# Kernel optimization log

Hardware: AMD Instinct MI355X
Metric: run time of the kernel (lower is better)

## Reference

```python
import jax, jax.numpy as jnp
import numpy as np

N_EMBED = 1024
HEAD_SIZE = 128

def setup_inputs() -> dict:
    key = jax.random.key(0)
    k1, k2, k3, k4 = jax.random.split(key, 4)
    x = jax.random.normal(k1, (8, 2048, N_EMBED), dtype=jnp.float32)
    # torch.nn.Linear default init: U(-1/sqrt(in), 1/sqrt(in)); stored as [out, in],
    # we store transposed [in, out] for x @ W.
    bound = 1.0 / np.sqrt(N_EMBED)
    Wk = jax.random.uniform(k2, (N_EMBED, HEAD_SIZE), jnp.float32, -bound, bound)
    Wq = jax.random.uniform(k3, (N_EMBED, HEAD_SIZE), jnp.float32, -bound, bound)
    Wv = jax.random.uniform(k4, (N_EMBED, HEAD_SIZE), jnp.float32, -bound, bound)
    return {"x": x, "Wk": Wk, "Wq": Wq, "Wv": Wv}

def reference(x, Wk, Wq, Wv):
    # x: [B, T, E]
    k = jnp.einsum('bte,eh->bth', x, Wk)  # [B, T, H]
    q = jnp.einsum('bte,eh->bth', x, Wq)
    v = jnp.einsum('bte,eh->bth', x, Wv)
    scale = 1.0 / np.sqrt(HEAD_SIZE).astype(np.float32)
    wei = jnp.einsum('bqh,bkh->bqk', q, k) * scale  # [B, T, T]
    wei = jax.nn.softmax(wei, axis=-1)
    out = jnp.einsum('bqk,bkh->bqh', wei, v)  # [B, T, H]
    return out
```

## Files before the change

### kernel.cpp

```cpp
#include <hip/hip_runtime.h>

#define BATCH 8
#define TLEN 2048
#define EMB 1024
#define HDIM 128
#define SCALE 0.08838834764831845f
#define NSPLIT 4

typedef _Float16 f16x8 __attribute__((ext_vector_type(8)));
typedef _Float16 f16x4 __attribute__((ext_vector_type(4)));
typedef float f32x4 __attribute__((ext_vector_type(4)));

static __device__ __forceinline__ f32x4 mfma16(f16x8 a, f16x8 b, f32x4 c) {
    return __builtin_amdgcn_mfma_f32_16x16x32_f16(a, b, c, 0, 0, 0);
}

__global__ void prep_w(const float* __restrict__ Wk, const float* __restrict__ Wq,
                       const float* __restrict__ Wv, _Float16* __restrict__ wtf) {
    int g = blockIdx.x * 256 + threadIdx.x;
    int lane = g & 63;
    int kstep = (g >> 6) & 31;
    int ntile = g >> 11;
    int n = ntile * 16 + (lane & 15);
    int sel = n >> 7;
    int h = n & 127;
    const float* W = (sel == 0) ? Wk : (sel == 1) ? Wq : Wv;
    int kbase = kstep * 32 + (lane >> 4) * 8;
    f16x8 o;
#pragma unroll
    for (int j = 0; j < 8; j++) {
        float v = W[(size_t)(kbase + j) * HDIM + h];
        if (sel == 1) v *= SCALE;
        o[j] = (_Float16)v;
    }
    *(f16x8*)&wtf[(size_t)g * 8] = o;
}

__global__ __launch_bounds__(256, 2) void proj_kernel(
        const float* __restrict__ x, const _Float16* __restrict__ wtf,
        _Float16* __restrict__ kb, _Float16* __restrict__ qb, _Float16* __restrict__ vbT) {
    __shared__ _Float16 xs[2][32 * 72];
    const int t = threadIdx.x;
    const int m0 = blockIdx.x * 32;
    const int wv = t >> 6;
    const int lane = t & 63;
    const int m16 = lane & 15;
    const int quad = lane >> 4;
    const int n0 = wv * 96;
    const int r0 = t >> 4;
    const int c0 = (t & 15) * 4;

    const f32x4 zero4 = {0.f, 0.f, 0.f, 0.f};
    f32x4 acc[2][6];
#pragma unroll
    for (int mt = 0; mt < 2; mt++)
#pragma unroll
        for (int nt = 0; nt < 6; nt++) acc[mt][nt] = zero4;

    const float* xrow0 = &x[(size_t)(m0 + r0) * EMB + c0];
    const float* xrow1 = &x[(size_t)(m0 + 16 + r0) * EMB + c0];

    float4 xv[2][2];
    f16x8 bf[2][12];
    xv[0][0] = *(const float4*)(xrow0);
    xv[0][1] = *(const float4*)(xrow1);
#pragma unroll
    for (int ks = 0; ks < 2; ks++)
#pragma unroll
        for (int nt = 0; nt < 6; nt++)
            bf[0][ks * 6 + nt] = *(const f16x8*)
                &wtf[((size_t)((wv * 6 + nt) * 32 + ks) * 64 + lane) * 8];

#pragma unroll
    for (int it = 0; it < 16; it++) {
        const int cur = it & 1, nxt = cur ^ 1;
#pragma unroll
        for (int i = 0; i < 2; i++) {
            f16x4 h;
            h[0] = (_Float16)xv[cur][i].x; h[1] = (_Float16)xv[cur][i].y;
            h[2] = (_Float16)xv[cur][i].z; h[3] = (_Float16)xv[cur][i].w;
            *(f16x4*)&xs[cur][(r0 + 16 * i) * 72 + c0] = h;
        }
        __syncthreads();
        if (it < 15) {
            xv[nxt][0] = *(const float4*)(xrow0 + (it + 1) * 64);
            xv[nxt][1] = *(const float4*)(xrow1 + (it + 1) * 64);
#pragma unroll
            for (int ks = 0; ks < 2; ks++)
#pragma unroll
                for (int nt = 0; nt < 6; nt++)
                    bf[nxt][ks * 6 + nt] = *(const f16x8*)
                        &wtf[((size_t)((wv * 6 + nt) * 32 + (it + 1) * 2 + ks) * 64 + lane) * 8];
        }
#pragma unroll
        for (int ks = 0; ks < 2; ks++) {
            f16x8 a0 = *(const f16x8*)&xs[cur][m16 * 72 + ks * 32 + quad * 8];
            f16x8 a1 = *(const f16x8*)&xs[cur][(16 + m16) * 72 + ks * 32 + quad * 8];
#pragma unroll
            for (int nt = 0; nt < 6; nt++) {
                acc[0][nt] = mfma16(a0, bf[cur][ks * 6 + nt], acc[0][nt]);
                acc[1][nt] = mfma16(a1, bf[cur][ks * 6 + nt], acc[1][nt]);
            }
        }
    }
#pragma unroll
    for (int nt = 0; nt < 6; nt++) {
        int n = n0 + nt * 16 + m16;
        int nsel = n >> 7;
        int h = n & 127;
        if (nsel < 2) {
            _Float16* dst = (nsel == 0) ? kb : qb;
#pragma unroll
            for (int mt = 0; mt < 2; mt++)
#pragma unroll
                for (int r = 0; r < 4; r++) {
                    int mg = m0 + mt * 16 + quad * 4 + r;
                    dst[(size_t)mg * HDIM + h] = (_Float16)acc[mt][nt][r];
                }
        } else {
#pragma unroll
            for (int mt = 0; mt < 2; mt++) {
                int mg = m0 + mt * 16 + quad * 4;
                int bb = mg >> 11, tok = mg & 2047;
                f16x4 pk;
#pragma unroll
                for (int r = 0; r < 4; r++) pk[r] = (_Float16)acc[mt][nt][r];
                *(f16x4*)&vbT[((size_t)bb * HDIM + h) * TLEN + tok] = pk;
            }
        }
    }
}

__global__ __launch_bounds__(256, 3) void attn_kernel(
        const _Float16* __restrict__ qb, const _Float16* __restrict__ kb,
        const _Float16* __restrict__ vbT,
        _Float16* __restrict__ po, float* __restrict__ pl) {
    __shared__ _Float16 kls[64 * 132];
    __shared__ _Float16 vtl[128 * 68];
    __shared__ _Float16 pls[4 * 32 * 72];
    const int t = threadIdx.x;
    const int qt = blockIdx.x;
    const int b = blockIdx.y;
    const int sp = blockIdx.z;
    const int wv = t >> 6;
    const int lane = t & 63;
    const int m16 = lane & 15;
    const int quad = lane >> 4;
    const int q0 = qt * 128 + wv * 32;
    _Float16* pw = pls + wv * (32 * 72);

    f16x8 qf[2][4];
#pragma unroll
    for (int mt = 0; mt < 2; mt++)
#pragma unroll
        for (int ks = 0; ks < 4; ks++)
            qf[mt][ks] = *(const f16x8*)
                &qb[((size_t)b * TLEN + q0 + mt * 16 + m16) * HDIM + ks * 32 + quad * 8];

    const f32x4 zero4 = {0.f, 0.f, 0.f, 0.f};
    f32x4 o[2][8];
    float lacc[2] = {0.f, 0.f};
#pragma unroll
    for (int mt = 0; mt < 2; mt++)
#pragma unroll
        for (int nt = 0; nt < 8; nt++) o[mt][nt] = zero4;

    for (int kt = sp * 8; kt < sp * 8 + 8; kt++) {
        const int k0 = kt * 64;
        f16x8 kreg[4];
#pragma unroll
        for (int rep = 0; rep < 4; rep++) {
            int u = t + rep * 256;
            kreg[rep] = *(const f16x8*)
                &kb[((size_t)b * TLEN + k0 + (u >> 4)) * HDIM + (u & 15) * 8];
        }
        __syncthreads();
#pragma unroll
        for (int rep = 0; rep < 4; rep++) {
            int u = t + rep * 256;
            *(f16x8*)&kls[(u >> 4) * 132 + (u & 15) * 8] = kreg[rep];
        }
#pragma unroll
        for (int rep = 0; rep < 4; rep++) {
            int u = t + rep * 256;
            f16x8 v = *(const f16x8*)
                &vbT[((size_t)b * HDIM + (u >> 3)) * TLEN + k0 + (u & 7) * 8];
            *(f16x8*)&vtl[(u >> 3) * 68 + (u & 7) * 8] = v;
        }
        __syncthreads();
#pragma unroll
        for (int kt_ = 0; kt_ < 4; kt_++) {
            f32x4 st0 = zero4, st1 = zero4;
#pragma unroll
            for (int ks = 0; ks < 4; ks++) {
                f16x8 kf = *(const f16x8*)&kls[(kt_ * 16 + m16) * 132 + ks * 32 + quad * 8];
                st0 = mfma16(kf, qf[0][ks], st0);
                st1 = mfma16(kf, qf[1][ks], st1);
            }
            f16x4 p0, p1;
#pragma unroll
            for (int r = 0; r < 4; r++) {
                float e0 = __expf(st0[r]);
                float e1 = __expf(st1[r]);
                lacc[0] += e0;
                lacc[1] += e1;
                p0[r] = (_Float16)e0;
                p1[r] = (_Float16)e1;
            }
            *(f16x4*)&pw[m16 * 72 + kt_ * 16 + quad * 4] = p0;
            *(f16x4*)&pw[(16 + m16) * 72 + kt_ * 16 + quad * 4] = p1;
        }
        f16x8 ap[2][2];
#pragma unroll
        for (int mt = 0; mt < 2; mt++)
#pragma unroll
            for (int kc = 0; kc < 2; kc++)
                ap[mt][kc] = *(const f16x8*)&pw[(mt * 16 + m16) * 72 + kc * 32 + quad * 8];
#pragma unroll
        for (int nt = 0; nt < 8; nt++) {
            f16x8 b0 = *(const f16x8*)&vtl[(nt * 16 + m16) * 68 + quad * 8];
            f16x8 b1 = *(const f16x8*)&vtl[(nt * 16 + m16) * 68 + 32 + quad * 8];
            o[0][nt] = mfma16(ap[0][0], b0, o[0][nt]);
            o[0][nt] = mfma16(ap[0][1], b1, o[0][nt]);
            o[1][nt] = mfma16(ap[1][0], b0, o[1][nt]);
            o[1][nt] = mfma16(ap[1][1], b1, o[1][nt]);
        }
    }
#pragma unroll
    for (int mt = 0; mt < 2; mt++) {
        lacc[mt] += __shfl_xor(lacc[mt], 16);
        lacc[mt] += __shfl_xor(lacc[mt], 32);
    }
#pragma unroll
    for (int mt = 0; mt < 2; mt++) {
        if (quad == 0)
            pl[((size_t)(sp * BATCH + b)) * TLEN + q0 + mt * 16 + m16] = lacc[mt];
#pragma unroll
        for (int r = 0; r < 4; r++) {
            int row = q0 + mt * 16 + quad * 4 + r;
            size_t prow = ((size_t)(sp * BATCH + b)) * TLEN + row;
#pragma unroll
            for (int nt = 0; nt < 8; nt++)
                po[prow * HDIM + nt * 16 + m16] = (_Float16)o[mt][nt][r];
        }
    }
}

__global__ void combine_kernel(const _Float16* __restrict__ po, const float* __restrict__ pl,
                               float* __restrict__ out) {
    int g = blockIdx.x * 256 + threadIdx.x;
    int row = g >> 5;
    int part = g & 31;
    int bb = row >> 11;
    int tok = row & 2047;
    float L = 0.f;
    float4 acc = {0.f, 0.f, 0.f, 0.f};
#pragma unroll
    for (int s = 0; s < NSPLIT; s++) {
        size_t prow = ((size_t)(s * BATCH + bb)) * TLEN + tok;
        L += pl[prow];
        f16x4 p = *(const f16x4*)&po[prow * HDIM + part * 4];
        acc.x += (float)p[0]; acc.y += (float)p[1];
        acc.z += (float)p[2]; acc.w += (float)p[3];
    }
    float inv = 1.f / L;
    float4 res = {acc.x * inv, acc.y * inv, acc.z * inv, acc.w * inv};
    *(float4*)&out[(size_t)row * HDIM + part * 4] = res;
}

extern "C" void kernel_launch(void* const* d_in, const int* in_sizes, int n_in,
                              void* d_out, int out_size, void* d_ws, size_t ws_size,
                              hipStream_t stream) {
    const float* x  = (const float*)d_in[0];
    const float* Wk = (const float*)d_in[1];
    const float* Wq = (const float*)d_in[2];
    const float* Wv = (const float*)d_in[3];
    float* out = (float*)d_out;
    char* ws = (char*)d_ws;
    _Float16* wtf = (_Float16*)(ws);
    _Float16* kb  = (_Float16*)(ws + (1ull << 20));
    _Float16* qb  = (_Float16*)(ws + (5ull << 20));
    _Float16* vbT = (_Float16*)(ws + (9ull << 20));
    _Float16* po  = (_Float16*)(ws + (13ull << 20));
    float* pl = (float*)(ws + (29ull << 20));

    prep_w<<<dim3(192), dim3(256), 0, stream>>>(Wk, Wq, Wv, wtf);
    proj_kernel<<<dim3(512), dim3(256), 0, stream>>>(x, wtf, kb, qb, vbT);
    attn_kernel<<<dim3(16, BATCH, NSPLIT), dim3(256), 0, stream>>>(qb, kb, vbT, po, pl);
    combine_kernel<<<dim3(2048), dim3(256), 0, stream>>>(po, pl, out);
}
```

Before: 159.3 us.

## Enlarge attention blocks to 512 queries, 64 per wave, with register-prefetched K/V

The attention kernel now uses 512-thread blocks that each cover 512 queries, with 64 query rows per wave instead of 32. Each K/V tile loaded into shared memory is therefore reused by four times as many queries. The key dimension is split 8 ways instead of 4, and the next K/V tile is prefetched into registers while the current one is being computed. The partial-output workspace doubles and the pl offset moves to fit it. The costs are higher register pressure (64 accumulator vectors per thread), fewer blocks, more combine traffic, and fewer key tiles per block to amortize setup.

```diff
diff --git a/kernel.cpp b/kernel.cpp
--- a/kernel.cpp
+++ b/kernel.cpp
@@ -5,7 +5,7 @@
 #define EMB 1024
 #define HDIM 128
 #define SCALE 0.08838834764831845f
-#define NSPLIT 4
+#define NSPLIT 8
 
 typedef _Float16 f16x8 __attribute__((ext_vector_type(8)));
 typedef _Float16 f16x4 __attribute__((ext_vector_type(4)));
@@ -131,13 +131,13 @@
     }
 }
 
-__global__ __launch_bounds__(256, 3) void attn_kernel(
+__global__ __launch_bounds__(512, 2) void attn_kernel(
         const _Float16* __restrict__ qb, const _Float16* __restrict__ kb,
         const _Float16* __restrict__ vbT,
         _Float16* __restrict__ po, float* __restrict__ pl) {
     __shared__ _Float16 kls[64 * 132];
     __shared__ _Float16 vtl[128 * 68];
-    __shared__ _Float16 pls[4 * 32 * 72];
+    __shared__ _Float16 pls[8 * 64 * 72];
     const int t = threadIdx.x;
     const int qt = blockIdx.x;
     const int b = blockIdx.y;
@@ -146,102 +146,108 @@
     const int lane = t & 63;
     const int m16 = lane & 15;
     const int quad = lane >> 4;
-    const int q0 = qt * 128 + wv * 32;
-    _Float16* pw = pls + wv * (32 * 72);
-
-    f16x8 qf[2][4];
-#pragma unroll
-    for (int mt = 0; mt < 2; mt++)
+    const int q0 = qt * 512 + wv * 64;
+    _Float16* pw = pls + wv * (64 * 72);
+
+    const _Float16* kbase = kb + (size_t)b * TLEN * HDIM;
+    const _Float16* vbase = vbT + (size_t)b * HDIM * TLEN;
+
+    f16x8 qf[4][4];
+#pragma unroll
+    for (int qs = 0; qs < 4; qs++)
 #pragma unroll
         for (int ks = 0; ks < 4; ks++)
-            qf[mt][ks] = *(const f16x8*)
-                &qb[((size_t)b * TLEN + q0 + mt * 16 + m16) * HDIM + ks * 32 + quad * 8];
+            qf[qs][ks] = *(const f16x8*)
+                &qb[((size_t)b * TLEN + q0 + qs * 16 + m16) * HDIM + ks * 32 + quad * 8];
 
     const f32x4 zero4 = {0.f, 0.f, 0.f, 0.f};
-    f32x4 o[2][8];
-    float lacc[2] = {0.f, 0.f};
-#pragma unroll
-    for (int mt = 0; mt < 2; mt++)
+    f32x4 o[4][8];
+    float lacc[4] = {0.f, 0.f, 0.f, 0.f};
+#pragma unroll
+    for (int mt = 0; mt < 4; mt++)
 #pragma unroll
         for (int nt = 0; nt < 8; nt++) o[mt][nt] = zero4;
 
-    for (int kt = sp * 8; kt < sp * 8 + 8; kt++) {
-        const int k0 = kt * 64;
-        f16x8 kreg[4];
-#pragma unroll
-        for (int rep = 0; rep < 4; rep++) {
-            int u = t + rep * 256;
-            kreg[rep] = *(const f16x8*)
-                &kb[((size_t)b * TLEN + k0 + (u >> 4)) * HDIM + (u & 15) * 8];
-        }
+    const int kt0 = sp * 4;
+    f16x8 kreg[2], vreg[2];
+#pragma unroll
+    for (int rep = 0; rep < 2; rep++) {
+        int u = t + rep * 512;
+        kreg[rep] = *(const f16x8*)&kbase[(size_t)(kt0 * 64 + (u >> 4)) * HDIM + (u & 15) * 8];
+        vreg[rep] = *(const f16x8*)&vbase[(size_t)(u >> 3) * TLEN + kt0 * 64 + (u & 7) * 8];
+    }
+
+    for (int it = 0; it < 4; it++) {
         __syncthreads();
 #pragma unroll
-        for (int rep = 0; rep < 4; rep++) {
-            int u = t + rep * 256;
+        for (int rep = 0; rep < 2; rep++) {
+            int u = t + rep * 512;
             *(f16x8*)&kls[(u >> 4) * 132 + (u & 15) * 8] = kreg[rep];
-        }
-#pragma unroll
-        for (int rep = 0; rep < 4; rep++) {
-            int u = t + rep * 256;
-            f16x8 v = *(const f16x8*)
-                &vbT[((size_t)b * HDIM + (u >> 3)) * TLEN + k0 + (u & 7) * 8];
-            *(f16x8*)&vtl[(u >> 3) * 68 + (u & 7) * 8] = v;
+            *(f16x8*)&vtl[(u >> 3) * 68 + (u & 7) * 8] = vreg[rep];
         }
         __syncthreads();
+        if (it < 3) {
+            const int k0n = (kt0 + it + 1) * 64;
+#pragma unroll
+            for (int rep = 0; rep < 2; rep++) {
+                int u = t + rep * 512;
+                kreg[rep] = *(const f16x8*)&kbase[(size_t)(k0n + (u >> 4)) * HDIM + (u & 15) * 8];
+                vreg[rep] = *(const f16x8*)&vbase[(size_t)(u >> 3) * TLEN + k0n + (u & 7) * 8];
+            }
+        }
 #pragma unroll
         for (int kt_ = 0; kt_ < 4; kt_++) {
-            f32x4 st0 = zero4, st1 = zero4;
+            f32x4 st[4] = {zero4, zero4, zero4, zero4};
 #pragma unroll
             for (int ks = 0; ks < 4; ks++) {
                 f16x8 kf = *(const f16x8*)&kls[(kt_ * 16 + m16) * 132 + ks * 32 + quad * 8];
-                st0 = mfma16(kf, qf[0][ks], st0);
-                st1 = mfma16(kf, qf[1][ks], st1);
-            }
-            f16x4 p0, p1;
-#pragma unroll
-            for (int r = 0; r < 4; r++) {
-                float e0 = __expf(st0[r]);
-                float e1 = __expf(st1[r]);
-                lacc[0] += e0;
-                lacc[1] += e1;
-                p0[r] = (_Float16)e0;
-                p1[r] = (_Float16)e1;
-            }
-            *(f16x4*)&pw[m16 * 72 + kt_ * 16 + quad * 4] = p0;
-            *(f16x4*)&pw[(16 + m16) * 72 + kt_ * 16 + quad * 4] = p1;
-        }
-        f16x8 ap[2][2];
-#pragma unroll
-        for (int mt = 0; mt < 2; mt++)
-#pragma unroll
-            for (int kc = 0; kc < 2; kc++)
-                ap[mt][kc] = *(const f16x8*)&pw[(mt * 16 + m16) * 72 + kc * 32 + quad * 8];
-#pragma unroll
-        for (int nt = 0; nt < 8; nt++) {
-            f16x8 b0 = *(const f16x8*)&vtl[(nt * 16 + m16) * 68 + quad * 8];
-            f16x8 b1 = *(const f16x8*)&vtl[(nt * 16 + m16) * 68 + 32 + quad * 8];
-            o[0][nt] = mfma16(ap[0][0], b0, o[0][nt]);
-            o[0][nt] = mfma16(ap[0][1], b1, o[0][nt]);
-            o[1][nt] = mfma16(ap[1][0], b0, o[1][nt]);
-            o[1][nt] = mfma16(ap[1][1], b1, o[1][nt]);
-        }
-    }
-#pragma unroll
-    for (int mt = 0; mt < 2; mt++) {
-        lacc[mt] += __shfl_xor(lacc[mt], 16);
-        lacc[mt] += __shfl_xor(lacc[mt], 32);
-    }
-#pragma unroll
-    for (int mt = 0; mt < 2; mt++) {
+#pragma unroll
+                for (int qs = 0; qs < 4; qs++)
+                    st[qs] = mfma16(kf, qf[qs][ks], st[qs]);
+            }
+#pragma unroll
+            for (int qs = 0; qs < 4; qs++) {
+                f16x4 p;
+#pragma unroll
+                for (int r = 0; r < 4; r++) {
+                    float e = __expf(st[qs][r]);
+                    lacc[qs] += e;
+                    p[r] = (_Float16)e;
+                }
+                *(f16x4*)&pw[(qs * 16 + m16) * 72 + kt_ * 16 + quad * 4] = p;
+            }
+        }
+#pragma unroll
+        for (int kc = 0; kc < 2; kc++) {
+            f16x8 ap[4];
+#pragma unroll
+            for (int mt = 0; mt < 4; mt++)
+                ap[mt] = *(const f16x8*)&pw[(mt * 16 + m16) * 72 + kc * 32 + quad * 8];
+#pragma unroll
+            for (int nt = 0; nt < 8; nt++) {
+                f16x8 bv = *(const f16x8*)&vtl[(nt * 16 + m16) * 68 + kc * 32 + quad * 8];
+#pragma unroll
+                for (int mt = 0; mt < 4; mt++)
+                    o[mt][nt] = mfma16(ap[mt], bv, o[mt][nt]);
+            }
+        }
+    }
+#pragma unroll
+    for (int qs = 0; qs < 4; qs++) {
+        lacc[qs] += __shfl_xor(lacc[qs], 16);
+        lacc[qs] += __shfl_xor(lacc[qs], 32);
+    }
+#pragma unroll
+    for (int qs = 0; qs < 4; qs++) {
         if (quad == 0)
-            pl[((size_t)(sp * BATCH + b)) * TLEN + q0 + mt * 16 + m16] = lacc[mt];
+            pl[((size_t)(sp * BATCH + b)) * TLEN + q0 + qs * 16 + m16] = lacc[qs];
 #pragma unroll
         for (int r = 0; r < 4; r++) {
-            int row = q0 + mt * 16 + quad * 4 + r;
+            int row = q0 + qs * 16 + quad * 4 + r;
             size_t prow = ((size_t)(sp * BATCH + b)) * TLEN + row;
 #pragma unroll
             for (int nt = 0; nt < 8; nt++)
-                po[prow * HDIM + nt * 16 + m16] = (_Float16)o[mt][nt][r];
+                po[prow * HDIM + nt * 16 + m16] = (_Float16)o[qs][nt][r];
         }
     }
 }
@@ -282,10 +288,10 @@
     _Float16* qb  = (_Float16*)(ws + (5ull << 20));
     _Float16* vbT = (_Float16*)(ws + (9ull << 20));
     _Float16* po  = (_Float16*)(ws + (13ull << 20));
-    float* pl = (float*)(ws + (29ull << 20));
+    float* pl = (float*)(ws + (45ull << 20));
 
     prep_w<<<dim3(192), dim3(256), 0, stream>>>(Wk, Wq, Wv, wtf);
     proj_kernel<<<dim3(512), dim3(256), 0, stream>>>(x, wtf, kb, qb, vbT);
-    attn_kernel<<<dim3(16, BATCH, NSPLIT), dim3(256), 0, stream>>>(qb, kb, vbT, po, pl);
+    attn_kernel<<<dim3(4, BATCH, NSPLIT), dim3(512), 0, stream>>>(qb, kb, vbT, po, pl);
     combine_kernel<<<dim3(2048), dim3(256), 0, stream>>>(po, pl, out);
 }
```

Measured after the change: 192.7 us. 20.9% more time.

## Raise key-split count to six and store partials in MFMA fragment layout

Applied to the files above, without the earlier changes.

Splits the key range across six partitions instead of four, giving 768 attention blocks for better CU fill on the 256-CU device, with uneven 5/6 tile ranges per split. Partial outputs are now written as packed f16x4 per lane in the MFMA accumulator layout rather than as scattered scalar halves. The combine kernel is rewritten to read that fragment layout and fetch row sums via shuffles. The cost is more partial traffic and combine work, plus imbalance between splits that get 5 or 6 tiles.

```diff
diff --git a/kernel.cpp b/kernel.cpp
--- a/kernel.cpp
+++ b/kernel.cpp
@@ -5,7 +5,7 @@
 #define EMB 1024
 #define HDIM 128
 #define SCALE 0.08838834764831845f
-#define NSPLIT 4
+#define NSPLIT 6
 
 typedef _Float16 f16x8 __attribute__((ext_vector_type(8)));
 typedef _Float16 f16x4 __attribute__((ext_vector_type(4)));
@@ -165,7 +165,9 @@
 #pragma unroll
         for (int nt = 0; nt < 8; nt++) o[mt][nt] = zero4;
 
-    for (int kt = sp * 8; kt < sp * 8 + 8; kt++) {
+    const int kt_beg = (sp * 32) / NSPLIT;
+    const int kt_end = ((sp + 1) * 32) / NSPLIT;
+    for (int kt = kt_beg; kt < kt_end; kt++) {
         const int k0 = kt * 64;
         f16x8 kreg[4];
 #pragma unroll
@@ -236,36 +238,46 @@
         if (quad == 0)
             pl[((size_t)(sp * BATCH + b)) * TLEN + q0 + mt * 16 + m16] = lacc[mt];
 #pragma unroll
-        for (int r = 0; r < 4; r++) {
-            int row = q0 + mt * 16 + quad * 4 + r;
-            size_t prow = ((size_t)(sp * BATCH + b)) * TLEN + row;
-#pragma unroll
-            for (int nt = 0; nt < 8; nt++)
-                po[prow * HDIM + nt * 16 + m16] = (_Float16)o[mt][nt][r];
+        for (int nt = 0; nt < 8; nt++) {
+            int fid = (((b * 16 + qt) * 4 + wv) * 2 + mt) * 8 + nt;
+            f16x4 pk;
+#pragma unroll
+            for (int r = 0; r < 4; r++) pk[r] = (_Float16)o[mt][nt][r];
+            *(f16x4*)&po[((size_t)(sp * 8192 + fid) * 64 + lane) * 4] = pk;
         }
     }
 }
 
 __global__ void combine_kernel(const _Float16* __restrict__ po, const float* __restrict__ pl,
                                float* __restrict__ out) {
-    int g = blockIdx.x * 256 + threadIdx.x;
-    int row = g >> 5;
-    int part = g & 31;
-    int bb = row >> 11;
-    int tok = row & 2047;
-    float L = 0.f;
-    float4 acc = {0.f, 0.f, 0.f, 0.f};
+    const int t = threadIdx.x;
+    const int u = blockIdx.x * 4 + (t >> 6);
+    const int lane = t & 63;
+    const int m16 = lane & 15;
+    const int quad = lane >> 4;
+    const int nt = u & 7;
+    const int rg = u >> 3;
+    const int mt = rg & 1;
+    const int wv = (rg >> 1) & 3;
+    const int qt = (rg >> 3) & 15;
+    const int b = rg >> 7;
+    const int rloc = qt * 128 + wv * 32 + mt * 16;
+    float Lr = 0.f;
+#pragma unroll
+    for (int s = 0; s < NSPLIT; s++)
+        Lr += pl[((size_t)(s * BATCH + b)) * TLEN + rloc + m16];
+    f32x4 acc = {0.f, 0.f, 0.f, 0.f};
 #pragma unroll
     for (int s = 0; s < NSPLIT; s++) {
-        size_t prow = ((size_t)(s * BATCH + bb)) * TLEN + tok;
-        L += pl[prow];
-        f16x4 p = *(const f16x4*)&po[prow * HDIM + part * 4];
-        acc.x += (float)p[0]; acc.y += (float)p[1];
-        acc.z += (float)p[2]; acc.w += (float)p[3];
-    }
-    float inv = 1.f / L;
-    float4 res = {acc.x * inv, acc.y * inv, acc.z * inv, acc.w * inv};
-    *(float4*)&out[(size_t)row * HDIM + part * 4] = res;
+        f16x4 p = *(const f16x4*)&po[((size_t)(s * 8192 + u) * 64 + lane) * 4];
+        acc[0] += (float)p[0]; acc[1] += (float)p[1];
+        acc[2] += (float)p[2]; acc[3] += (float)p[3];
+    }
+#pragma unroll
+    for (int r = 0; r < 4; r++) {
+        float L = __shfl(Lr, quad * 4 + r);
+        out[((size_t)b * TLEN + rloc + quad * 4 + r) * HDIM + nt * 16 + m16] = acc[r] / L;
+    }
 }
 
 extern "C" void kernel_launch(void* const* d_in, const int* in_sizes, int n_in,
@@ -282,7 +294,7 @@
     _Float16* qb  = (_Float16*)(ws + (5ull << 20));
     _Float16* vbT = (_Float16*)(ws + (9ull << 20));
     _Float16* po  = (_Float16*)(ws + (13ull << 20));
-    float* pl = (float*)(ws + (29ull << 20));
+    float* pl = (float*)(ws + (45ull << 20));
 
     prep_w<<<dim3(192), dim3(256), 0, stream>>>(Wk, Wq, Wv, wtf);
     proj_kernel<<<dim3(512), dim3(256), 0, stream>>>(x, wtf, kb, qb, vbT);
```

New measurement: 156.7 us (median of 2 runs). Within noise of the previous version (-1.6%).
